# Kernel tuning notes

Hardware: AMD Instinct MI355X
Metric: run time of the kernel (lower is better)

The kernel has to match this reference:

```python
import jax, jax.numpy as jnp
import numpy as np

C = 0.01          # curvature
EPS = 1e-6        # eps used in midpoint / weight normalization (matches torch code)
MIN_NORM = 1e-10  # numerical floor for norms
BALL_EPS = 1e-5   # projection margin


def _norm(x):
    return jnp.sqrt(jnp.clip(jnp.sum(x * x, axis=-1, keepdims=True), MIN_NORM))


def log_map_zero(x, c):
    sc = jnp.sqrt(c)
    n = _norm(x)
    return jnp.arctanh(jnp.clip(sc * n, -1.0 + BALL_EPS, 1.0 - BALL_EPS)) * x / (sc * n)


def exp_map_zero(v, c):
    sc = jnp.sqrt(c)
    n = _norm(v)
    return jnp.tanh(sc * n) * v / (sc * n)


def project_to_ball(x, c):
    n = _norm(x)
    maxn = (1.0 - BALL_EPS) / jnp.sqrt(c)
    return jnp.where(n > maxn, x * (maxn / n), x)


def mobius_add(x, y, c):
    x2 = jnp.sum(x * x, axis=-1, keepdims=True)
    y2 = jnp.sum(y * y, axis=-1, keepdims=True)
    xy = jnp.sum(x * y, axis=-1, keepdims=True)
    num = (1.0 + 2.0 * c * xy + c * y2) * x + (1.0 - c * x2) * y
    den = 1.0 + 2.0 * c * xy + (c * c) * x2 * y2
    return num / jnp.clip(den, MIN_NORM)


def setup_inputs() -> dict:
    N, E, R, D = 50000, 400000, 230, 16
    key = jax.random.key(0)
    ks = jax.random.split(key, 8)
    h_hyper = project_to_ball(0.1 * jax.random.normal(ks[0], (N, D), dtype=jnp.float32), C)
    node_norm = jax.random.uniform(ks[1], (N, 1), dtype=jnp.float32)
    xav = float(np.sqrt(2.0 / (D + D)))
    rel_weight = xav * jax.random.normal(ks[2], (R, D, D), dtype=jnp.float32)
    loop_weight = xav * jax.random.normal(ks[3], (D, D), dtype=jnp.float32)
    rel_emb = 0.1 * jax.random.normal(ks[4], (R, D), dtype=jnp.float32)
    src = jax.random.randint(ks[5], (E,), 0, N, dtype=jnp.int32)
    dst = jax.random.randint(ks[6], (E,), 0, N, dtype=jnp.int32)
    etype = jax.random.randint(ks[7], (E,), 0, R, dtype=jnp.int32)
    return {"h_hyper": h_hyper, "node_norm": node_norm, "rel_weight": rel_weight,
            "loop_weight": loop_weight, "rel_emb": rel_emb,
            "src": src, "dst": dst, "etype": etype}


def reference(h_hyper, node_norm, rel_weight, loop_weight, rel_emb, src, dst, etype):
    c = C
    N = h_hyper.shape[0]
    # --- msg_func: Mobius matvec per edge (log -> gathered GEMM -> +rel -> exp) ---
    h_tan = log_map_zero(h_hyper, c)                                  # [N, D]
    msg_tan = jnp.einsum('ei,eio->eo', h_tan[src], rel_weight[etype])  # [E, D]
    msg_tan = msg_tan + rel_emb[etype]
    msg = exp_map_zero(msg_tan, c)                                    # [E, D]
    # --- reduce_func: Einstein midpoint per destination node ---
    en = node_norm[dst, 0]                                            # [E] per-edge dst norm
    norm_sum = jax.ops.segment_sum(en, dst, num_segments=N)           # [N]
    w = en / (norm_sum[dst] + EPS)                                    # normalized weights
    lam = 2.0 / (1.0 - c * jnp.sum(msg * msg, axis=-1) + EPS)         # Lorentz factors [E]
    wl = w * lam
    numer = jax.ops.segment_sum(wl[:, None] * msg, dst, num_segments=N)  # [N, D]
    denom = jax.ops.segment_sum(wl, dst, num_segments=N) + EPS           # [N]
    h_agg = project_to_ball(numer / denom[:, None], c)
    # --- self loop in tangent space, combined with Mobius addition ---
    loop_hyp = exp_map_zero(h_tan @ loop_weight, c)
    h_new = mobius_add(h_agg, loop_hyp, c)
    return h_new
```

## Files before the change

### kernel.cpp

```cpp
#include <hip/hip_runtime.h>

#define C_CURV   0.01f
#define SQRT_C   0.1f
#define EPS_W    1e-6f
#define MIN_NORM 1e-10f
#define BALL_EPS 1e-5f
#define CAP      64
#define WSTRIDE  130

typedef __attribute__((ext_vector_type(4))) float f32x4;

__device__ __forceinline__ float fast_rcp(float x)  { return __builtin_amdgcn_rcpf(x); }
__device__ __forceinline__ float fast_sqrt(float x) { return __builtin_amdgcn_sqrtf(x); }
__device__ __forceinline__ float tanh_over_x(float x) {
    float t = __expf(2.0f * x);
    return (t - 1.0f) * fast_rcp((t + 1.0f) * x);
}
__device__ __forceinline__ unsigned bf16_rne(float x) {
    unsigned u = __float_as_uint(x);
    return (u + 0x7FFFu + ((u >> 16) & 1u)) >> 16;
}

__device__ __forceinline__ float group4_sum(float v) {
    v += __shfl_xor(v, 1, 64);
    v += __shfl_xor(v, 2, 64);
    return v;
}

__global__ __launch_bounds__(256) void fhnn_zero(int* __restrict__ cursor, int n4) {
    int i = blockIdx.x * blockDim.x + threadIdx.x;
    if (i < n4) ((int4*)cursor)[i] = make_int4(0, 0, 0, 0);
}

__global__ __launch_bounds__(256) void fhnn_prep(
        const float* __restrict__ h_hyper,
        const float* __restrict__ loop_weight,
        const int*   __restrict__ src,
        const int*   __restrict__ dst,
        const int*   __restrict__ etype,
        float* __restrict__ h_tan,
        float* __restrict__ loop_hyp,
        int*      __restrict__ cursor,
        unsigned* __restrict__ bucket,
        int N, int E, int blocksN) {
    if ((int)blockIdx.x >= blocksN) {
        int e = (blockIdx.x - blocksN) * blockDim.x + threadIdx.x;
        if (e >= E) return;
        int t = dst[e];
        int slot = atomicAdd(&cursor[t], 1);
        if (slot < CAP)
            bucket[(size_t)t * CAP + slot] = (unsigned)src[e] | ((unsigned)etype[e] << 16);
        return;
    }
    __shared__ float Wl[256];
    Wl[threadIdx.x] = loop_weight[threadIdx.x];
    __syncthreads();

    int gid = blockIdx.x * blockDim.x + threadIdx.x;
    int t = gid >> 2, j = gid & 3;
    if (t >= N) return;

    f32x4 x = ((const f32x4*)h_hyper)[gid];

    float sq  = group4_sum(x.x * x.x + x.y * x.y + x.z * x.z + x.w * x.w);
    float n   = fast_sqrt(fmaxf(sq, MIN_NORM));
    float scn = SQRT_C * n;
    float z   = fminf(scn, 1.0f - BALL_EPS);
    float at  = 0.5f * __logf((1.0f + z) * fast_rcp(1.0f - z));
    float s   = at * fast_rcp(scn);
    f32x4 ht  = x * s;
    ((f32x4*)h_tan)[gid] = ht;

    f32x4 acc = (f32x4)(0.0f);
    #pragma unroll
    for (int q = 0; q < 4; ++q) {
        float h0 = __shfl(ht.x, q, 4);
        float h1 = __shfl(ht.y, q, 4);
        float h2 = __shfl(ht.z, q, 4);
        float h3 = __shfl(ht.w, q, 4);
        const f32x4* Wrow = (const f32x4*)Wl;
        acc += h0 * Wrow[(4 * q + 0) * 4 + j];
        acc += h1 * Wrow[(4 * q + 1) * 4 + j];
        acc += h2 * Wrow[(4 * q + 2) * 4 + j];
        acc += h3 * Wrow[(4 * q + 3) * 4 + j];
    }
    float sq2  = group4_sum(acc.x * acc.x + acc.y * acc.y + acc.z * acc.z + acc.w * acc.w);
    float n2   = fast_sqrt(fmaxf(sq2, MIN_NORM));
    float f2   = tanh_over_x(SQRT_C * n2);
    ((f32x4*)loop_hyp)[gid] = acc * f2;
}

__global__ __launch_bounds__(1024, 1) void fhnn_reduce(
        const float*    __restrict__ h_tan,
        const float*    __restrict__ rel_weight,
        const float*    __restrict__ rel_emb,
        const unsigned* __restrict__ bucket,
        const int*      __restrict__ cursor,
        const float*    __restrict__ node_norm,
        const float*    __restrict__ loop_hyp,
        float*          __restrict__ out,
        int N, int R) {
    extern __shared__ unsigned lds_w[];
    const int relOff = ((R * WSTRIDE + 3) & ~3);
    float* relE = (float*)(lds_w + relOff);

    const int totalW = R * 128;
    for (int idx = threadIdx.x; idx < totalW; idx += blockDim.x) {
        int r = idx >> 7, c = idx & 127;
        float a = rel_weight[r * 256 + 2 * c];
        float b = rel_weight[r * 256 + 2 * c + 1];
        lds_w[r * WSTRIDE + c] = bf16_rne(a) | (bf16_rne(b) << 16);
    }
    for (int idx = threadIdx.x; idx < R * 16; idx += blockDim.x)
        relE[idx] = rel_emb[idx];
    __syncthreads();

    int wv   = threadIdx.x >> 6;
    int lane = threadIdx.x & 63;
    int grp  = lane >> 4;
    int slot = (lane >> 2) & 3;
    int j    = lane & 3;

    for (int base = blockIdx.x * 64; base < N; base += gridDim.x * 64) {
        int t = base + wv * 4 + grp;
        if (t >= N) continue;

        int cn = min(cursor[t], CAP);

        f32x4 accM = (f32x4)(0.0f);
        float accL = 0.0f;
        for (int k = slot; k < cn; k += 4) {
            unsigned pk = bucket[(size_t)t * CAP + k];
            int s = (int)(pk & 0xFFFFu);
            int r = (int)(pk >> 16);

            const f32x4* h4 = (const f32x4*)(h_tan + (size_t)s * 16);
            f32x4 h0 = h4[0], h1 = h4[1], h2 = h4[2], h3 = h4[3];

            const unsigned* Ws = lds_w + (unsigned)r * WSTRIDE + 2u * (unsigned)j;
            f32x4 a4 = (f32x4)(0.0f);
            #define WSTEP(HS, I) { \
                uint2 w = *(const uint2*)(Ws + 8 * (I)); \
                f32x4 wvv; \
                wvv.x = __uint_as_float(w.x << 16); \
                wvv.y = __uint_as_float(w.x & 0xFFFF0000u); \
                wvv.z = __uint_as_float(w.y << 16); \
                wvv.w = __uint_as_float(w.y & 0xFFFF0000u); \
                a4 += (HS) * wvv; }
            WSTEP(h0.x,  0) WSTEP(h0.y,  1) WSTEP(h0.z,  2) WSTEP(h0.w,  3)
            WSTEP(h1.x,  4) WSTEP(h1.y,  5) WSTEP(h1.z,  6) WSTEP(h1.w,  7)
            WSTEP(h2.x,  8) WSTEP(h2.y,  9) WSTEP(h2.z, 10) WSTEP(h2.w, 11)
            WSTEP(h3.x, 12) WSTEP(h3.y, 13) WSTEP(h3.z, 14) WSTEP(h3.w, 15)
            #undef WSTEP

            f32x4 v = a4 + *(const f32x4*)(relE + r * 16 + 4 * j);

            float sq = group4_sum(v.x * v.x + v.y * v.y + v.z * v.z + v.w * v.w);
            float f  = tanh_over_x(SQRT_C * fast_sqrt(fmaxf(sq, MIN_NORM)));
            float m2 = f * f * sq;
            float lam = 2.0f * fast_rcp(1.0f - C_CURV * m2 + EPS_W);
            accM += v * (f * lam);
            accL += lam;
        }
        #pragma unroll
        for (int m = 4; m <= 8; m <<= 1) {
            accM.x += __shfl_xor(accM.x, m, 64);
            accM.y += __shfl_xor(accM.y, m, 64);
            accM.z += __shfl_xor(accM.z, m, 64);
            accM.w += __shfl_xor(accM.w, m, 64);
            accL   += __shfl_xor(accL,   m, 64);
        }

        float en    = node_norm[t];
        float wsc   = en * fast_rcp((float)cn * en + EPS_W);
        float denom = wsc * accL + EPS_W;
        float rs    = wsc * fast_rcp(denom);
        f32x4 x     = accM * rs;

        float x2 = group4_sum(x.x * x.x + x.y * x.y + x.z * x.z + x.w * x.w);
        float n  = fast_sqrt(fmaxf(x2, MIN_NORM));
        const float maxn = (1.0f - BALL_EPS) / SQRT_C;
        float scale = (n > maxn) ? (maxn * fast_rcp(n)) : 1.0f;
        x *= scale;

        f32x4 y   = ((const f32x4*)(loop_hyp + (size_t)t * 16))[j];
        float x2p = group4_sum(x.x * x.x + x.y * x.y + x.z * x.z + x.w * x.w);
        float y2  = group4_sum(y.x * y.x + y.y * y.y + y.z * y.z + y.w * y.w);
        float xy  = group4_sum(x.x * y.x + x.y * y.y + x.z * y.z + x.w * y.w);

        float a1  = 1.0f + 2.0f * C_CURV * xy + C_CURV * y2;
        float b1  = 1.0f - C_CURV * x2p;
        f32x4 num = a1 * x + b1 * y;
        float d2  = 1.0f + 2.0f * C_CURV * xy + C_CURV * C_CURV * x2p * y2;
        if (slot == 0)
            ((f32x4*)out)[t * 4 + j] = num * fast_rcp(fmaxf(d2, MIN_NORM));
    }
}

extern "C" void kernel_launch(void* const* d_in, const int* in_sizes, int n_in,
                              void* d_out, int out_size, void* d_ws, size_t ws_size,
                              hipStream_t stream) {
    const float* h_hyper     = (const float*)d_in[0];
    const float* node_norm   = (const float*)d_in[1];
    const float* rel_weight  = (const float*)d_in[2];
    const float* loop_weight = (const float*)d_in[3];
    const float* rel_emb     = (const float*)d_in[4];
    const int*   src         = (const int*)d_in[5];
    const int*   dst         = (const int*)d_in[6];
    const int*   etype       = (const int*)d_in[7];

    const int N = in_sizes[1];
    const int E = in_sizes[5];
    const int R = in_sizes[2] / 256;

    char* ws = (char*)d_ws;
    size_t offs = 0;
    auto alloc = [&](size_t bytes) -> void* {
        void* p = ws + offs;
        offs += (bytes + 255) & ~(size_t)255;
        return p;
    };
    float*    h_tan    = (float*)alloc((size_t)N * 16 * 4);
    float*    loop_hyp = (float*)alloc((size_t)N * 16 * 4);
    unsigned* bucket   = (unsigned*)alloc((size_t)N * CAP * 4);
    int*      cursor   = (int*)alloc((size_t)N * 4);
    int nZero4 = (N + 3) >> 2;

    int relOff   = ((R * WSTRIDE + 3) & ~3);
    int ldsBytes = (relOff + R * 16) * 4;
    hipFuncSetAttribute((const void*)fhnn_reduce,
                        hipFuncAttributeMaxDynamicSharedMemorySize, ldsBytes);

    const int threads = 256;
    int blocksZ  = (nZero4 + threads - 1) / threads;
    int blocksN4 = (N * 4 + threads - 1) / threads;
    int blocksE1 = (E + threads - 1) / threads;
    int blocksR  = 256;

    fhnn_zero<<<blocksZ, threads, 0, stream>>>(cursor, nZero4);
    fhnn_prep<<<blocksN4 + blocksE1, threads, 0, stream>>>(
        h_hyper, loop_weight, src, dst, etype, h_tan, loop_hyp, cursor, bucket,
        N, E, blocksN4);
    fhnn_reduce<<<blocksR, 1024, ldsBytes, stream>>>(
        h_tan, rel_weight, rel_emb, bucket, cursor, node_norm, loop_hyp,
        (float*)d_out, N, R);
}
```

Before: 66.65 us.

## Fuse zero, prep, and reduce into one cooperative kernel with grid syncs

Replaces the three kernel launches (cursor zeroing, prep/bucketing, reduce) with a single cooperative kernel of 256 blocks by 1024 threads that uses grid.sync between phases. This removes launch overhead and inter-kernel gaps, and overlaps the LDS weight staging with the earlier phases. In exchange, the prep and bucketing phases now run on only 256 persistent blocks with grid-stride loops instead of many small blocks. Node prep and edge bucketing are also serialized by an extra grid barrier, where before they ran in the same launch.

```diff
diff --git a/kernel.cpp b/kernel.cpp
--- a/kernel.cpp
+++ b/kernel.cpp
@@ -1,4 +1,7 @@
 #include <hip/hip_runtime.h>
+#include <hip/hip_cooperative_groups.h>
+
+namespace cg = cooperative_groups;
 
 #define C_CURV   0.01f
 #define SQRT_C   0.1f
@@ -20,180 +23,176 @@
     unsigned u = __float_as_uint(x);
     return (u + 0x7FFFu + ((u >> 16) & 1u)) >> 16;
 }
-
 __device__ __forceinline__ float group4_sum(float v) {
     v += __shfl_xor(v, 1, 64);
     v += __shfl_xor(v, 2, 64);
     return v;
 }
 
-__global__ __launch_bounds__(256) void fhnn_zero(int* __restrict__ cursor, int n4) {
-    int i = blockIdx.x * blockDim.x + threadIdx.x;
-    if (i < n4) ((int4*)cursor)[i] = make_int4(0, 0, 0, 0);
-}
-
-__global__ __launch_bounds__(256) void fhnn_prep(
+__global__ __launch_bounds__(1024, 1) void fhnn_fused(
         const float* __restrict__ h_hyper,
+        const float* __restrict__ node_norm,
+        const float* __restrict__ rel_weight,
         const float* __restrict__ loop_weight,
+        const float* __restrict__ rel_emb,
         const int*   __restrict__ src,
         const int*   __restrict__ dst,
         const int*   __restrict__ etype,
-        float* __restrict__ h_tan,
-        float* __restrict__ loop_hyp,
+        float*    __restrict__ h_tan,
+        float*    __restrict__ loop_hyp,
+        unsigned* __restrict__ bucket,
         int*      __restrict__ cursor,
-        unsigned* __restrict__ bucket,
-        int N, int E, int blocksN) {
-    if ((int)blockIdx.x >= blocksN) {
-        int e = (blockIdx.x - blocksN) * blockDim.x + threadIdx.x;
-        if (e >= E) return;
+        float*    __restrict__ out,
+        int N, int E, int R, int nZero4) {
+    extern __shared__ unsigned lds_w[];
+    const int relOff = ((R * WSTRIDE + 3) & ~3);
+    float* relE = (float*)(lds_w + relOff);
+    float* Wl   = (float*)(lds_w + relOff + R * 16);
+
+    cg::grid_group grid = cg::this_grid();
+
+    const int tid  = threadIdx.x;
+    const int gtid = blockIdx.x * blockDim.x + tid;
+    const int gthreads = gridDim.x * blockDim.x;
+
+    for (int i = gtid; i < nZero4; i += gthreads)
+        ((int4*)cursor)[i] = make_int4(0, 0, 0, 0);
+
+    for (int idx = tid; idx < R * 128; idx += blockDim.x) {
+        int r = idx >> 7, c = idx & 127;
+        float a = rel_weight[r * 256 + 2 * c];
+        float b = rel_weight[r * 256 + 2 * c + 1];
+        lds_w[r * WSTRIDE + c] = bf16_rne(a) | (bf16_rne(b) << 16);
+    }
+    for (int idx = tid; idx < R * 16; idx += blockDim.x)
+        relE[idx] = rel_emb[idx];
+    if (tid < 256) Wl[tid] = loop_weight[tid];
+    __syncthreads();
+
+    for (int gid = gtid; gid < N * 4; gid += gthreads) {
+        int t = gid >> 2, j = gid & 3;
+        (void)t;
+        f32x4 x = ((const f32x4*)h_hyper)[gid];
+
+        float sq  = group4_sum(x.x * x.x + x.y * x.y + x.z * x.z + x.w * x.w);
+        float n   = fast_sqrt(fmaxf(sq, MIN_NORM));
+        float scn = SQRT_C * n;
+        float z   = fminf(scn, 1.0f - BALL_EPS);
+        float at  = 0.5f * __logf((1.0f + z) * fast_rcp(1.0f - z));
+        float s   = at * fast_rcp(scn);
+        f32x4 ht  = x * s;
+        ((f32x4*)h_tan)[gid] = ht;
+
+        f32x4 acc = (f32x4)(0.0f);
+        #pragma unroll
+        for (int q = 0; q < 4; ++q) {
+            float h0 = __shfl(ht.x, q, 4);
+            float h1 = __shfl(ht.y, q, 4);
+            float h2 = __shfl(ht.z, q, 4);
+            float h3 = __shfl(ht.w, q, 4);
+            const f32x4* Wrow = (const f32x4*)Wl;
+            acc += h0 * Wrow[(4 * q + 0) * 4 + j];
+            acc += h1 * Wrow[(4 * q + 1) * 4 + j];
+            acc += h2 * Wrow[(4 * q + 2) * 4 + j];
+            acc += h3 * Wrow[(4 * q + 3) * 4 + j];
+        }
+        float sq2 = group4_sum(acc.x * acc.x + acc.y * acc.y + acc.z * acc.z + acc.w * acc.w);
+        float n2  = fast_sqrt(fmaxf(sq2, MIN_NORM));
+        float f2  = tanh_over_x(SQRT_C * n2);
+        ((f32x4*)loop_hyp)[gid] = acc * f2;
+    }
+
+    grid.sync();
+
+    for (int e = gtid; e < E; e += gthreads) {
         int t = dst[e];
         int slot = atomicAdd(&cursor[t], 1);
         if (slot < CAP)
             bucket[(size_t)t * CAP + slot] = (unsigned)src[e] | ((unsigned)etype[e] << 16);
-        return;
-    }
-    __shared__ float Wl[256];
-    Wl[threadIdx.x] = loop_weight[threadIdx.x];
-    __syncthreads();
-
-    int gid = blockIdx.x * blockDim.x + threadIdx.x;
-    int t = gid >> 2, j = gid & 3;
-    if (t >= N) return;
-
-    f32x4 x = ((const f32x4*)h_hyper)[gid];
-
-    float sq  = group4_sum(x.x * x.x + x.y * x.y + x.z * x.z + x.w * x.w);
-    float n   = fast_sqrt(fmaxf(sq, MIN_NORM));
-    float scn = SQRT_C * n;
-    float z   = fminf(scn, 1.0f - BALL_EPS);
-    float at  = 0.5f * __logf((1.0f + z) * fast_rcp(1.0f - z));
-    float s   = at * fast_rcp(scn);
-    f32x4 ht  = x * s;
-    ((f32x4*)h_tan)[gid] = ht;
-
-    f32x4 acc = (f32x4)(0.0f);
-    #pragma unroll
-    for (int q = 0; q < 4; ++q) {
-        float h0 = __shfl(ht.x, q, 4);
-        float h1 = __shfl(ht.y, q, 4);
-        float h2 = __shfl(ht.z, q, 4);
-        float h3 = __shfl(ht.w, q, 4);
-        const f32x4* Wrow = (const f32x4*)Wl;
-        acc += h0 * Wrow[(4 * q + 0) * 4 + j];
-        acc += h1 * Wrow[(4 * q + 1) * 4 + j];
-        acc += h2 * Wrow[(4 * q + 2) * 4 + j];
-        acc += h3 * Wrow[(4 * q + 3) * 4 + j];
-    }
-    float sq2  = group4_sum(acc.x * acc.x + acc.y * acc.y + acc.z * acc.z + acc.w * acc.w);
-    float n2   = fast_sqrt(fmaxf(sq2, MIN_NORM));
-    float f2   = tanh_over_x(SQRT_C * n2);
-    ((f32x4*)loop_hyp)[gid] = acc * f2;
-}
-
-__global__ __launch_bounds__(1024, 1) void fhnn_reduce(
-        const float*    __restrict__ h_tan,
-        const float*    __restrict__ rel_weight,
-        const float*    __restrict__ rel_emb,
-        const unsigned* __restrict__ bucket,
-        const int*      __restrict__ cursor,
-        const float*    __restrict__ node_norm,
-        const float*    __restrict__ loop_hyp,
-        float*          __restrict__ out,
-        int N, int R) {
-    extern __shared__ unsigned lds_w[];
-    const int relOff = ((R * WSTRIDE + 3) & ~3);
-    float* relE = (float*)(lds_w + relOff);
-
-    const int totalW = R * 128;
-    for (int idx = threadIdx.x; idx < totalW; idx += blockDim.x) {
-        int r = idx >> 7, c = idx & 127;
-        float a = rel_weight[r * 256 + 2 * c];
-        float b = rel_weight[r * 256 + 2 * c + 1];
-        lds_w[r * WSTRIDE + c] = bf16_rne(a) | (bf16_rne(b) << 16);
-    }
-    for (int idx = threadIdx.x; idx < R * 16; idx += blockDim.x)
-        relE[idx] = rel_emb[idx];
-    __syncthreads();
-
-    int wv   = threadIdx.x >> 6;
-    int lane = threadIdx.x & 63;
-    int grp  = lane >> 4;
-    int slot = (lane >> 2) & 3;
-    int j    = lane & 3;
-
-    for (int base = blockIdx.x * 64; base < N; base += gridDim.x * 64) {
-        int t = base + wv * 4 + grp;
-        if (t >= N) continue;
-
-        int cn = min(cursor[t], CAP);
-
-        f32x4 accM = (f32x4)(0.0f);
-        float accL = 0.0f;
-        for (int k = slot; k < cn; k += 4) {
-            unsigned pk = bucket[(size_t)t * CAP + k];
-            int s = (int)(pk & 0xFFFFu);
-            int r = (int)(pk >> 16);
-
-            const f32x4* h4 = (const f32x4*)(h_tan + (size_t)s * 16);
-            f32x4 h0 = h4[0], h1 = h4[1], h2 = h4[2], h3 = h4[3];
-
-            const unsigned* Ws = lds_w + (unsigned)r * WSTRIDE + 2u * (unsigned)j;
-            f32x4 a4 = (f32x4)(0.0f);
-            #define WSTEP(HS, I) { \
-                uint2 w = *(const uint2*)(Ws + 8 * (I)); \
-                f32x4 wvv; \
-                wvv.x = __uint_as_float(w.x << 16); \
-                wvv.y = __uint_as_float(w.x & 0xFFFF0000u); \
-                wvv.z = __uint_as_float(w.y << 16); \
-                wvv.w = __uint_as_float(w.y & 0xFFFF0000u); \
-                a4 += (HS) * wvv; }
-            WSTEP(h0.x,  0) WSTEP(h0.y,  1) WSTEP(h0.z,  2) WSTEP(h0.w,  3)
-            WSTEP(h1.x,  4) WSTEP(h1.y,  5) WSTEP(h1.z,  6) WSTEP(h1.w,  7)
-            WSTEP(h2.x,  8) WSTEP(h2.y,  9) WSTEP(h2.z, 10) WSTEP(h2.w, 11)
-            WSTEP(h3.x, 12) WSTEP(h3.y, 13) WSTEP(h3.z, 14) WSTEP(h3.w, 15)
-            #undef WSTEP
-
-            f32x4 v = a4 + *(const f32x4*)(relE + r * 16 + 4 * j);
-
-            float sq = group4_sum(v.x * v.x + v.y * v.y + v.z * v.z + v.w * v.w);
-            float f  = tanh_over_x(SQRT_C * fast_sqrt(fmaxf(sq, MIN_NORM)));
-            float m2 = f * f * sq;
-            float lam = 2.0f * fast_rcp(1.0f - C_CURV * m2 + EPS_W);
-            accM += v * (f * lam);
-            accL += lam;
+    }
+
+    grid.sync();
+
+    {
+        int wv   = tid >> 6;
+        int lane = tid & 63;
+        int grp  = lane >> 4;
+        int slot = (lane >> 2) & 3;
+        int j    = lane & 3;
+        int wstart = (blockIdx.x * 16 + wv) * 4 + grp;
+        int nstride = gridDim.x * 16 * 4;
+
+        for (int t = wstart; t < N; t += nstride) {
+            int cn = min(cursor[t], CAP);
+
+            f32x4 accM = (f32x4)(0.0f);
+            float accL = 0.0f;
+            for (int k = slot; k < cn; k += 4) {
+                unsigned pk = bucket[(size_t)t * CAP + k];
+                int s = (int)(pk & 0xFFFFu);
+                int r = (int)(pk >> 16);
+
+                const f32x4* h4 = (const f32x4*)(h_tan + (size_t)s * 16);
+                f32x4 h0 = h4[0], h1 = h4[1], h2 = h4[2], h3 = h4[3];
+
+                const unsigned* Ws = lds_w + (unsigned)r * WSTRIDE + 2u * (unsigned)j;
+                f32x4 a4 = (f32x4)(0.0f);
+                #define WSTEP(HS, I) { \
+                    uint2 w = *(const uint2*)(Ws + 8 * (I)); \
+                    f32x4 wvv; \
+                    wvv.x = __uint_as_float(w.x << 16); \
+                    wvv.y = __uint_as_float(w.x & 0xFFFF0000u); \
+                    wvv.z = __uint_as_float(w.y << 16); \
+                    wvv.w = __uint_as_float(w.y & 0xFFFF0000u); \
+                    a4 += (HS) * wvv; }
+                WSTEP(h0.x,  0) WSTEP(h0.y,  1) WSTEP(h0.z,  2) WSTEP(h0.w,  3)
+                WSTEP(h1.x,  4) WSTEP(h1.y,  5) WSTEP(h1.z,  6) WSTEP(h1.w,  7)
+                WSTEP(h2.x,  8) WSTEP(h2.y,  9) WSTEP(h2.z, 10) WSTEP(h2.w, 11)
+                WSTEP(h3.x, 12) WSTEP(h3.y, 13) WSTEP(h3.z, 14) WSTEP(h3.w, 15)
+                #undef WSTEP
+
+                f32x4 v = a4 + *(const f32x4*)(relE + r * 16 + 4 * j);
+
+                float sq = group4_sum(v.x * v.x + v.y * v.y + v.z * v.z + v.w * v.w);
+                float f  = tanh_over_x(SQRT_C * fast_sqrt(fmaxf(sq, MIN_NORM)));
+                float m2 = f * f * sq;
+                float lam = 2.0f * fast_rcp(1.0f - C_CURV * m2 + EPS_W);
+                accM += v * (f * lam);
+                accL += lam;
+            }
+            #pragma unroll
+            for (int m = 4; m <= 8; m <<= 1) {
+                accM.x += __shfl_xor(accM.x, m, 64);
+                accM.y += __shfl_xor(accM.y, m, 64);
+                accM.z += __shfl_xor(accM.z, m, 64);
+                accM.w += __shfl_xor(accM.w, m, 64);
+                accL   += __shfl_xor(accL,   m, 64);
+            }
+
+            float en    = node_norm[t];
+            float wsc   = en * fast_rcp((float)cn * en + EPS_W);
+            float denom = wsc * accL + EPS_W;
+            float rs    = wsc * fast_rcp(denom);
+            f32x4 x     = accM * rs;
+
+            float x2 = group4_sum(x.x * x.x + x.y * x.y + x.z * x.z + x.w * x.w);
+            float n  = fast_sqrt(fmaxf(x2, MIN_NORM));
+            const float maxn = (1.0f - BALL_EPS) / SQRT_C;
+            float scale = (n > maxn) ? (maxn * fast_rcp(n)) : 1.0f;
+            x *= scale;
+
+            f32x4 y   = ((const f32x4*)(loop_hyp + (size_t)t * 16))[j];
+            float x2p = group4_sum(x.x * x.x + x.y * x.y + x.z * x.z + x.w * x.w);
+            float y2  = group4_sum(y.x * y.x + y.y * y.y + y.z * y.z + y.w * y.w);
+            float xy  = group4_sum(x.x * y.x + x.y * y.y + x.z * y.z + x.w * y.w);
+
+            float a1  = 1.0f + 2.0f * C_CURV * xy + C_CURV * y2;
+            float b1  = 1.0f - C_CURV * x2p;
+            f32x4 num = a1 * x + b1 * y;
+            float d2  = 1.0f + 2.0f * C_CURV * xy + C_CURV * C_CURV * x2p * y2;
+            if (slot == 0)
+                ((f32x4*)out)[t * 4 + j] = num * fast_rcp(fmaxf(d2, MIN_NORM));
         }
-        #pragma unroll
-        for (int m = 4; m <= 8; m <<= 1) {
-            accM.x += __shfl_xor(accM.x, m, 64);
-            accM.y += __shfl_xor(accM.y, m, 64);
-            accM.z += __shfl_xor(accM.z, m, 64);
-            accM.w += __shfl_xor(accM.w, m, 64);
-            accL   += __shfl_xor(accL,   m, 64);
-        }
-
-        float en    = node_norm[t];
-        float wsc   = en * fast_rcp((float)cn * en + EPS_W);
-        float denom = wsc * accL + EPS_W;
-        float rs    = wsc * fast_rcp(denom);
-        f32x4 x     = accM * rs;
-
-        float x2 = group4_sum(x.x * x.x + x.y * x.y + x.z * x.z + x.w * x.w);
-        float n  = fast_sqrt(fmaxf(x2, MIN_NORM));
-        const float maxn = (1.0f - BALL_EPS) / SQRT_C;
-        float scale = (n > maxn) ? (maxn * fast_rcp(n)) : 1.0f;
-        x *= scale;
-
-        f32x4 y   = ((const f32x4*)(loop_hyp + (size_t)t * 16))[j];
-        float x2p = group4_sum(x.x * x.x + x.y * x.y + x.z * x.z + x.w * x.w);
-        float y2  = group4_sum(y.x * y.x + y.y * y.y + y.z * y.z + y.w * y.w);
-        float xy  = group4_sum(x.x * y.x + x.y * y.y + x.z * y.z + x.w * y.w);
-
-        float a1  = 1.0f + 2.0f * C_CURV * xy + C_CURV * y2;
-        float b1  = 1.0f - C_CURV * x2p;
-        f32x4 num = a1 * x + b1 * y;
-        float d2  = 1.0f + 2.0f * C_CURV * xy + C_CURV * C_CURV * x2p * y2;
-        if (slot == 0)
-            ((f32x4*)out)[t * 4 + j] = num * fast_rcp(fmaxf(d2, MIN_NORM));
     }
 }
 
@@ -209,9 +208,9 @@
     const int*   dst         = (const int*)d_in[6];
     const int*   etype       = (const int*)d_in[7];
 
-    const int N = in_sizes[1];
-    const int E = in_sizes[5];
-    const int R = in_sizes[2] / 256;
+    int N = in_sizes[1];
+    int E = in_sizes[5];
+    int R = in_sizes[2] / 256;
 
     char* ws = (char*)d_ws;
     size_t offs = 0;
@@ -227,21 +226,17 @@
     int nZero4 = (N + 3) >> 2;
 
     int relOff   = ((R * WSTRIDE + 3) & ~3);
-    int ldsBytes = (relOff + R * 16) * 4;
-    hipFuncSetAttribute((const void*)fhnn_reduce,
+    int ldsBytes = (relOff + R * 16 + 256) * 4;
+    hipFuncSetAttribute((const void*)fhnn_fused,
                         hipFuncAttributeMaxDynamicSharedMemorySize, ldsBytes);
 
-    const int threads = 256;
-    int blocksZ  = (nZero4 + threads - 1) / threads;
-    int blocksN4 = (N * 4 + threads - 1) / threads;
-    int blocksE1 = (E + threads - 1) / threads;
-    int blocksR  = 256;
-
-    fhnn_zero<<<blocksZ, threads, 0, stream>>>(cursor, nZero4);
-    fhnn_prep<<<blocksN4 + blocksE1, threads, 0, stream>>>(
-        h_hyper, loop_weight, src, dst, etype, h_tan, loop_hyp, cursor, bucket,
-        N, E, blocksN4);
-    fhnn_reduce<<<blocksR, 1024, ldsBytes, stream>>>(
-        h_tan, rel_weight, rel_emb, bucket, cursor, node_norm, loop_hyp,
-        (float*)d_out, N, R);
-}
+    float* outp = (float*)d_out;
+    void* args[] = {
+        (void*)&h_hyper, (void*)&node_norm, (void*)&rel_weight, (void*)&loop_weight,
+        (void*)&rel_emb, (void*)&src, (void*)&dst, (void*)&etype,
+        (void*)&h_tan, (void*)&loop_hyp, (void*)&bucket, (void*)&cursor,
+        (void*)&outp, (void*)&N, (void*)&E, (void*)&R, (void*)&nZero4
+    };
+    hipLaunchCooperativeKernel((const void*)fhnn_fused, dim3(256), dim3(1024),
+                               args, ldsBytes, stream);
+}
```

Result: slower. 140.1 us (+110.2%).
